# Kernel optimization log

Hardware: AMD Instinct MI355X
Metric: run time of the kernel (lower is better)

The kernel has to match this reference:

```python
import jax, jax.numpy as jnp
import numpy as np

B, T, I = 8, 8192, 512
E, K, J = 16, 1024, 512

def setup_inputs() -> dict:
    key = jax.random.key(0)
    k1, k2, k3 = jax.random.split(key, 3)
    x = jax.random.normal(k1, (B, T, I), dtype=jnp.float32)
    Ind = jax.random.randint(k2, (B, E, K), 0, T, dtype=jnp.int32)
    bound = 1.0 / np.sqrt(I)
    W = jax.random.uniform(k3, (E, I, J), dtype=jnp.float32, minval=-bound, maxval=bound)
    return {"x": x, "Ind": Ind, "W": W}

def reference(x, Ind, W):
    # gather: [B,E,K,I] = x[b, Ind[b,e,k], :]
    gathered = jnp.take_along_axis(x[:, None, :, :], Ind[:, :, :, None], axis=2)
    # per-expert GEMM: [B,E,K,J]
    return jnp.einsum('beki,eij->bekj', gathered, W)
```

## Files before the change

kernel.cpp:

```cpp
#include <hip/hip_runtime.h>
#include <stdint.h>

typedef short short8 __attribute__((ext_vector_type(8)));
typedef float floatx16 __attribute__((ext_vector_type(16)));

constexpr int CB = 8;
constexpr int CT = 8192;
constexpr int CI = 512;
constexpr int CE = 16;
constexpr int CK = 1024;
constexpr int CJ = 512;

__device__ uint32_t g_xb[(size_t)CB * CT * CI / 2];
__device__ uint32_t g_wb[(size_t)CE * CI * CJ / 2];

__device__ __forceinline__ uint32_t f2bf(float f) {
    union { float f; uint32_t u; } c; c.f = f;
    return (c.u + 0x7fffu + ((c.u >> 16) & 1u)) >> 16;
}
__device__ __forceinline__ uint32_t pack2(float lo, float hi) {
    return f2bf(lo) | (f2bf(hi) << 16);
}

__device__ __forceinline__ void gl_lds16(const uint32_t* g, uint32_t* l) {
    __builtin_amdgcn_global_load_lds(
        (const __attribute__((address_space(1))) uint32_t*)g,
        (__attribute__((address_space(3))) uint32_t*)l,
        16, 0, 0);
}

__global__ __launch_bounds__(256) void cvt_x(const float* __restrict__ x,
                                             uint32_t* __restrict__ xb) {
    size_t i = (size_t)blockIdx.x * 256 + threadIdx.x;
    const float4* src = (const float4*)x;
    float4 a = src[2 * i], b = src[2 * i + 1];
    ((uint4*)xb)[i] = make_uint4(pack2(a.x, a.y), pack2(a.z, a.w),
                                 pack2(b.x, b.y), pack2(b.z, b.w));
}

__global__ __launch_bounds__(256) void cvt_w(const float* __restrict__ W,
                                             uint32_t* __restrict__ wb) {
    uint32_t tid = blockIdx.x * 256 + threadIdx.x;
    int jn  = tid & 127;
    int kpq = (tid >> 7) & 7;
    int kt  = (tid >> 10) & 7;
    int nt  = (tid >> 13) & 3;
    int e   = tid >> 15;
    int n   = nt * 128 + jn;
    int k0  = kt * 64 + kpq * 8;
    const float* src = W + ((size_t)e * CI + k0) * CJ + n;
    uint4 o;
    o.x = pack2(src[0 * CJ], src[1 * CJ]);
    o.y = pack2(src[2 * CJ], src[3 * CJ]);
    o.z = pack2(src[4 * CJ], src[5 * CJ]);
    o.w = pack2(src[6 * CJ], src[7 * CJ]);
    ((uint4*)wb)[tid] = o;
}

__global__ __launch_bounds__(256, 4) void eg_kernel(
    const uint32_t* __restrict__ xb, const int* __restrict__ Ind,
    const uint32_t* __restrict__ wb, float* __restrict__ out)
{
    __shared__ __align__(16) uint32_t As[128 * 32];
    __shared__ __align__(16) uint32_t Bs[32 * 128];
    __shared__ int s_idx[128];

    const int t = threadIdx.x;
    const int z = blockIdx.z;
    const int e = z & (CE - 1);
    const int b = z >> 4;
    const int mtile = blockIdx.y;
    const int ntile = blockIdx.x;

    if (t < 128) s_idx[t] = Ind[z * CK + mtile * 128 + t];
    __syncthreads();

    const int ln = t & 63, wv = t >> 6;

    const int sr = ln >> 3;
    const int gchunk = (ln & 7) ^ sr;
    const uint32_t* xb_b = xb + (size_t)b * CT * 256;
    const uint32_t* pA[4];
    #pragma unroll
    for (int i = 0; i < 4; ++i) {
        int r = wv * 32 + i * 8 + sr;
        pA[i] = xb_b + (size_t)s_idx[r] * 256 + gchunk * 4;
    }
    const uint32_t* pB = wb + ((size_t)(e * 4 + ntile) * 8) * 4096 + wv * 1024 + ln * 4;

    const int wm = (wv >> 1) * 64, wn = (wv & 1) * 64;
    const int lrow = ln & 31;
    const int lh = ln >> 5;

    const floatx16 fz = {0.f,0.f,0.f,0.f,0.f,0.f,0.f,0.f,0.f,0.f,0.f,0.f,0.f,0.f,0.f,0.f};
    floatx16 acc[2][2] = {{fz, fz}, {fz, fz}};

    for (int kt = 0; kt < 8; ++kt) {
        #pragma unroll
        for (int i = 0; i < 4; ++i)
            gl_lds16(pA[i] + kt * 32, &As[wv * 1024 + i * 256]);
        #pragma unroll
        for (int i = 0; i < 4; ++i)
            gl_lds16(pB + (size_t)kt * 4096 + i * 256, &Bs[wv * 1024 + i * 256]);
        __syncthreads();

        #pragma unroll
        for (int s = 0; s < 4; ++s) {
            short8 af[2], bfr[2];
            #pragma unroll
            for (int mt = 0; mt < 2; ++mt) {
                const int row = wm + mt * 32 + lrow;
                const int ch = (s * 2 + lh) ^ (lrow & 7);
                af[mt] = *(const short8*)&As[row * 32 + ch * 4];
            }
            #pragma unroll
            for (int nt = 0; nt < 2; ++nt) {
                const int jn = wn + nt * 32 + lrow;
                bfr[nt] = *(const short8*)&Bs[(s * 2 + lh) * 512 + jn * 4];
            }
            #pragma unroll
            for (int mt = 0; mt < 2; ++mt)
                #pragma unroll
                for (int nt = 0; nt < 2; ++nt)
                    acc[mt][nt] = __builtin_amdgcn_mfma_f32_32x32x16_bf16(
                        af[mt], bfr[nt], acc[mt][nt], 0, 0, 0);
        }
        __syncthreads();
    }

    const size_t obase = (size_t)z * CK * CJ;
    #pragma unroll
    for (int mt = 0; mt < 2; ++mt) {
        const int gm0 = mtile * 128 + wm + mt * 32 + lh * 4;
        #pragma unroll
        for (int nt = 0; nt < 2; ++nt) {
            const int gn = ntile * 128 + wn + nt * 32 + lrow;
            #pragma unroll
            for (int r = 0; r < 16; ++r) {
                const int gm = gm0 + (r & 3) + 8 * (r >> 2);
                out[obase + (size_t)gm * CJ + gn] = acc[mt][nt][r];
            }
        }
    }
}

extern "C" void kernel_launch(void* const* d_in, const int* in_sizes, int n_in,
                              void* d_out, int out_size, void* d_ws, size_t ws_size,
                              hipStream_t stream) {
    const float* x   = (const float*)d_in[0];
    const int*   Ind = (const int*)d_in[1];
    const float* W   = (const float*)d_in[2];
    float* out = (float*)d_out;

    uint32_t* xb; hipGetSymbolAddress((void**)&xb, HIP_SYMBOL(g_xb));
    uint32_t* wb; hipGetSymbolAddress((void**)&wb, HIP_SYMBOL(g_wb));

    hipLaunchKernelGGL(cvt_x, dim3(CB * CT * CI / 8 / 256), dim3(256), 0, stream, x, xb);
    hipLaunchKernelGGL(cvt_w, dim3(CE * CI * CJ / 8 / 256), dim3(256), 0, stream, W, wb);

    dim3 grid(CJ / 128, CK / 128, CB * CE);
    hipLaunchKernelGGL(eg_kernel, grid, dim3(256), 0, stream, xb, Ind, wb, out);
}
```

Before: 477.6 us.

## Double-buffer LDS tiles in gather GEMM and fuse conversion kernels

Splits the K loop into ping-pong LDS buffers so the global-to-LDS loads for the next K tile are issued before the MFMA work on the current tile, hiding load latency. The x and W bf16 conversion kernels are merged into one launch to remove a launch boundary. The occupancy hint drops from 4 to 2 blocks per CU because LDS use doubles. This may reduce latency hiding from concurrent blocks.

```diff
diff --git a/kernel.cpp b/kernel.cpp
--- a/kernel.cpp
+++ b/kernel.cpp
@@ -29,40 +29,80 @@
         16, 0, 0);
 }
 
-__global__ __launch_bounds__(256) void cvt_x(const float* __restrict__ x,
-                                             uint32_t* __restrict__ xb) {
-    size_t i = (size_t)blockIdx.x * 256 + threadIdx.x;
-    const float4* src = (const float4*)x;
-    float4 a = src[2 * i], b = src[2 * i + 1];
-    ((uint4*)xb)[i] = make_uint4(pack2(a.x, a.y), pack2(a.z, a.w),
-                                 pack2(b.x, b.y), pack2(b.z, b.w));
+constexpr int XBLK = CB * CT * CI / 8 / 256;
+constexpr int WBLK = CE * CI * CJ / 8 / 256;
+__global__ __launch_bounds__(256) void cvt_xw(
+    const float* __restrict__ x, uint32_t* __restrict__ xb,
+    const float* __restrict__ W, uint32_t* __restrict__ wb)
+{
+    const int bid = blockIdx.x;
+    if (bid < XBLK) {
+        size_t i = (size_t)bid * 256 + threadIdx.x;
+        const float4* src = (const float4*)x;
+        float4 a = src[2 * i], b = src[2 * i + 1];
+        ((uint4*)xb)[i] = make_uint4(pack2(a.x, a.y), pack2(a.z, a.w),
+                                     pack2(b.x, b.y), pack2(b.z, b.w));
+    } else {
+        uint32_t tid = (uint32_t)(bid - XBLK) * 256 + threadIdx.x;
+        int jn  = tid & 127;
+        int kpq = (tid >> 7) & 7;
+        int kt  = (tid >> 10) & 7;
+        int nt  = (tid >> 13) & 3;
+        int e   = tid >> 15;
+        int n   = nt * 128 + jn;
+        int k0  = kt * 64 + kpq * 8;
+        const float* src = W + ((size_t)e * CI + k0) * CJ + n;
+        uint4 o;
+        o.x = pack2(src[0 * CJ], src[1 * CJ]);
+        o.y = pack2(src[2 * CJ], src[3 * CJ]);
+        o.z = pack2(src[4 * CJ], src[5 * CJ]);
+        o.w = pack2(src[6 * CJ], src[7 * CJ]);
+        ((uint4*)wb)[tid] = o;
+    }
 }
 
-__global__ __launch_bounds__(256) void cvt_w(const float* __restrict__ W,
-                                             uint32_t* __restrict__ wb) {
-    uint32_t tid = blockIdx.x * 256 + threadIdx.x;
-    int jn  = tid & 127;
-    int kpq = (tid >> 7) & 7;
-    int kt  = (tid >> 10) & 7;
-    int nt  = (tid >> 13) & 3;
-    int e   = tid >> 15;
-    int n   = nt * 128 + jn;
-    int k0  = kt * 64 + kpq * 8;
-    const float* src = W + ((size_t)e * CI + k0) * CJ + n;
-    uint4 o;
-    o.x = pack2(src[0 * CJ], src[1 * CJ]);
-    o.y = pack2(src[2 * CJ], src[3 * CJ]);
-    o.z = pack2(src[4 * CJ], src[5 * CJ]);
-    o.w = pack2(src[6 * CJ], src[7 * CJ]);
-    ((uint4*)wb)[tid] = o;
+__device__ __forceinline__ void stage_tiles(const uint32_t* const* pA, const uint32_t* pB,
+                                            int kt, uint32_t* As, uint32_t* Bs, int wv) {
+    #pragma unroll
+    for (int i = 0; i < 4; ++i)
+        gl_lds16(pA[i] + kt * 32, &As[wv * 1024 + i * 256]);
+    #pragma unroll
+    for (int i = 0; i < 4; ++i)
+        gl_lds16(pB + (size_t)kt * 4096 + i * 256, &Bs[wv * 1024 + i * 256]);
 }
 
-__global__ __launch_bounds__(256, 4) void eg_kernel(
+__device__ __forceinline__ void compute_tile(const uint32_t* As, const uint32_t* Bs,
+                                             int wm, int wn, int lrow, int lh,
+                                             floatx16 acc[2][2]) {
+    #pragma unroll
+    for (int s = 0; s < 4; ++s) {
+        short8 af[2], bfr[2];
+        #pragma unroll
+        for (int mt = 0; mt < 2; ++mt) {
+            const int row = wm + mt * 32 + lrow;
+            const int ch = (s * 2 + lh) ^ (lrow & 7);
+            af[mt] = *(const short8*)&As[row * 32 + ch * 4];
+        }
+        #pragma unroll
+        for (int nt = 0; nt < 2; ++nt) {
+            const int jn = wn + nt * 32 + lrow;
+            bfr[nt] = *(const short8*)&Bs[(s * 2 + lh) * 512 + jn * 4];
+        }
+        #pragma unroll
+        for (int mt = 0; mt < 2; ++mt)
+            #pragma unroll
+            for (int nt = 0; nt < 2; ++nt)
+                acc[mt][nt] = __builtin_amdgcn_mfma_f32_32x32x16_bf16(
+                    af[mt], bfr[nt], acc[mt][nt], 0, 0, 0);
+    }
+}
+
+__global__ __launch_bounds__(256, 2) void eg_kernel(
     const uint32_t* __restrict__ xb, const int* __restrict__ Ind,
     const uint32_t* __restrict__ wb, float* __restrict__ out)
 {
-    __shared__ __align__(16) uint32_t As[128 * 32];
-    __shared__ __align__(16) uint32_t Bs[32 * 128];
+    __shared__ __align__(16) uint32_t As0[128 * 32], As1[128 * 32];
+    __shared__ __align__(16) uint32_t Bs0[32 * 128], Bs1[32 * 128];
     __shared__ int s_idx[128];
 
     const int t = threadIdx.x;
@@ -95,36 +135,16 @@
     const floatx16 fz = {0.f,0.f,0.f,0.f,0.f,0.f,0.f,0.f,0.f,0.f,0.f,0.f,0.f,0.f,0.f,0.f};
     floatx16 acc[2][2] = {{fz, fz}, {fz, fz}};
 
-    for (int kt = 0; kt < 8; ++kt) {
-        #pragma unroll
-        for (int i = 0; i < 4; ++i)
-            gl_lds16(pA[i] + kt * 32, &As[wv * 1024 + i * 256]);
-        #pragma unroll
-        for (int i = 0; i < 4; ++i)
-            gl_lds16(pB + (size_t)kt * 4096 + i * 256, &Bs[wv * 1024 + i * 256]);
+    stage_tiles(pA, pB, 0, As0, Bs0, wv);
+    __syncthreads();
+    #pragma unroll
+    for (int ktp = 0; ktp < 4; ++ktp) {
+        stage_tiles(pA, pB, 2 * ktp + 1, As1, Bs1, wv);
+        compute_tile(As0, Bs0, wm, wn, lrow, lh, acc);
         __syncthreads();
-
-        #pragma unroll
-        for (int s = 0; s < 4; ++s) {
-            short8 af[2], bfr[2];
-            #pragma unroll
-            for (int mt = 0; mt < 2; ++mt) {
-                const int row = wm + mt * 32 + lrow;
-                const int ch = (s * 2 + lh) ^ (lrow & 7);
-                af[mt] = *(const short8*)&As[row * 32 + ch * 4];
-            }
-            #pragma unroll
-            for (int nt = 0; nt < 2; ++nt) {
-                const int jn = wn + nt * 32 + lrow;
-                bfr[nt] = *(const short8*)&Bs[(s * 2 + lh) * 512 + jn * 4];
-            }
-            #pragma unroll
-            for (int mt = 0; mt < 2; ++mt)
-                #pragma unroll
-                for (int nt = 0; nt < 2; ++nt)
-                    acc[mt][nt] = __builtin_amdgcn_mfma_f32_32x32x16_bf16(
-                        af[mt], bfr[nt], acc[mt][nt], 0, 0, 0);
-        }
+        if (ktp < 3)
+            stage_tiles(pA, pB, 2 * ktp + 2, As0, Bs0, wv);
+        compute_tile(As1, Bs1, wm, wn, lrow, lh, acc);
         __syncthreads();
     }
 
@@ -155,8 +175,7 @@
     uint32_t* xb; hipGetSymbolAddress((void**)&xb, HIP_SYMBOL(g_xb));
     uint32_t* wb; hipGetSymbolAddress((void**)&wb, HIP_SYMBOL(g_wb));
 
-    hipLaunchKernelGGL(cvt_x, dim3(CB * CT * CI / 8 / 256), dim3(256), 0, stream, x, xb);
-    hipLaunchKernelGGL(cvt_w, dim3(CE * CI * CJ / 8 / 256), dim3(256), 0, stream, W, wb);
+    hipLaunchKernelGGL(cvt_xw, dim3(XBLK + WBLK), dim3(256), 0, stream, x, xb, W, wb);
 
     dim3 grid(CJ / 128, CK / 128, CB * CE);
     hipLaunchKernelGGL(eg_kernel, grid, dim3(256), 0, stream, xb, Ind, wb, out);
```

Result: no change. 473.5 us (-0.9%).
